# Optimization experiments

Hardware: AMD Instinct MI355X
Metric: run time of the kernel (lower is better)

Reference implementation:

```python
import jax, jax.numpy as jnp
import numpy as np

N_NODES = 50000
N_EDGES = 800000
N_FEAT = 256


def setup_inputs() -> dict:
    key = jax.random.key(0)
    k_h, k_src, k_dst, k_w1, k_w2 = jax.random.split(key, 5)
    h = jax.random.normal(k_h, (N_NODES, N_FEAT), dtype=jnp.float32)
    src = jax.random.randint(k_src, (N_EDGES,), 0, N_NODES, dtype=jnp.int32)
    dst = jax.random.randint(k_dst, (N_EDGES,), 0, N_NODES, dtype=jnp.int32)
    # Kaiming-uniform-ish init like nn.Linear defaults
    b1 = 1.0 / np.sqrt(2 * N_FEAT)
    b2 = 1.0 / np.sqrt(N_FEAT)
    W1_w = jax.random.uniform(k_w1, (N_FEAT, 2 * N_FEAT), dtype=jnp.float32, minval=-b1, maxval=b1)
    W1_b = jnp.zeros((N_FEAT,), dtype=jnp.float32)
    W2_w = jax.random.uniform(k_w2, (1, N_FEAT), dtype=jnp.float32, minval=-b2, maxval=b2)
    W2_b = jnp.zeros((1,), dtype=jnp.float32)
    return {"h": h, "src": src, "dst": dst, "W1_w": W1_w, "W1_b": W1_b, "W2_w": W2_w, "W2_b": W2_b}


def reference(h, src, dst, W1_w, W1_b, W2_w, W2_b):
    # Gather per-edge endpoint features and concat along feature dim: [E, 2F]
    e = jnp.concatenate([h[src], h[dst]], axis=-1)
    # 2-layer MLP: Linear -> ReLU -> Linear, squeeze to per-edge score [E]
    hid = jax.nn.relu(e @ W1_w.T + W1_b)          # [E, F]
    score = (hid @ W2_w.T + W2_b)[:, 0]            # [E]
    return score
```

## Files before the change

### kernel.cpp

```cpp
#include <hip/hip_runtime.h>

#define F 256
#define TWO_F 512
#define BM 128
#define BN 64
#define BK 64

typedef __attribute__((ext_vector_type(8))) short short8;
typedef __attribute__((ext_vector_type(4))) float float4v;

static __device__ __forceinline__ unsigned short f2bf(float f) {
    unsigned u = __float_as_uint(f);
    u += 0x7FFFu + ((u >> 16) & 1u);
    return (unsigned short)(u >> 16);
}
static __device__ __forceinline__ unsigned pack2(float lo, float hi) {
    unsigned a = __float_as_uint(lo) + 0x8000u;
    unsigned b = __float_as_uint(hi) + 0x8000u;
    return __builtin_amdgcn_perm(b, a, 0x07060302u);
}
static __device__ __forceinline__ float blo(unsigned u) { return __uint_as_float(u << 16); }
static __device__ __forceinline__ float rawf(unsigned u) { return __uint_as_float(u); }

__global__ __launch_bounds__(256) void prep_kernel(
    const float* __restrict__ h, const float* __restrict__ W1,
    unsigned short* __restrict__ hb, unsigned short* __restrict__ Wb, int M)
{
    int i = blockIdx.x * blockDim.x + threadIdx.x;
    if (i < M * 128) {
        int m = i >> 7;
        int kp = (i & 127) * 2;
        float2 v = *(const float2*)(h + (size_t)m * F + kp);
        unsigned pk = pack2(v.x, v.y);
        int ksw = ((kp & 63) + (m & 7) * 8) & 63;
        *(unsigned*)(hb + (size_t)m * F + (kp & ~63) + ksw) = pk;
    }
    if (i < TWO_F * F) {
        int n = i >> 8;
        int k = i & 255;
        float v = W1[(n & 255) * TWO_F + ((n >> 8) << 8) + k];
        int kin_sw = ((k & 63) + (n & 7) * 8) & 63;
        Wb[n * F + (k & ~63) + kin_sw] = f2bf(v);
    }
}

__global__ __launch_bounds__(256, 4) void gemm_kernel(
    const unsigned short* __restrict__ hb, const unsigned short* __restrict__ Wb,
    const float* __restrict__ b1v, unsigned short* __restrict__ C, int M)
{
    __shared__ unsigned short sA[BM * BK];
    __shared__ unsigned short sB[BN * BK];

    const int ib = blockIdx.x;
    const int r8 = ib & 7;
    const int q  = ib >> 3;
    const int by = q & 7;
    const int bx = (q >> 3) * 8 + r8;
    const int bm = bx * BM;
    if (bm >= M) return;
    const int bn = by * BN;

    const int tid  = threadIdx.x;
    const int lane = tid & 63;
    const int wid  = tid >> 6;
    const int st_r = lane >> 3;
    const int st_k = (lane & 7) * 8;
    const int quad = lane >> 4;
    const int l15  = lane & 15;
    const int rot  = (l15 & 7) * 8;

    float4v acc[2][4];
    #pragma unroll
    for (int i = 0; i < 2; ++i)
        #pragma unroll
        for (int j = 0; j < 4; ++j) acc[i][j] = (float4v)(0.f);

    for (int k0 = 0; k0 < F; k0 += BK) {
        #pragma unroll
        for (int p = 0; p < 4; ++p) {
            int r = wid * 32 + p * 8;
            int am = bm + r + st_r; if (am > M - 1) am = M - 1;
            const unsigned short* ga = hb + (size_t)am * F + k0 + st_k;
            __builtin_amdgcn_global_load_lds(
                (const __attribute__((address_space(1))) unsigned int*)ga,
                (__attribute__((address_space(3))) unsigned int*)&sA[r * BK],
                16, 0, 0);
        }
        #pragma unroll
        for (int p = 0; p < 2; ++p) {
            int r = wid * 16 + p * 8;
            const unsigned short* gb = Wb + (size_t)(bn + r + st_r) * F + k0 + st_k;
            __builtin_amdgcn_global_load_lds(
                (const __attribute__((address_space(1))) unsigned int*)gb,
                (__attribute__((address_space(3))) unsigned int*)&sB[r * BK],
                16, 0, 0);
        }
        __syncthreads();

        #pragma unroll
        for (int ks = 0; ks < 2; ++ks) {
            const int koff = (ks * 32 + quad * 8 + rot) & 63;
            short8 afr[2], bfr[4];
            #pragma unroll
            for (int mt = 0; mt < 2; ++mt)
                afr[mt] = *(const short8*)&sA[(wid * 32 + mt * 16 + l15) * BK + koff];
            #pragma unroll
            for (int nt = 0; nt < 4; ++nt)
                bfr[nt] = *(const short8*)&sB[(nt * 16 + l15) * BK + koff];
            #pragma unroll
            for (int mt = 0; mt < 2; ++mt)
                #pragma unroll
                for (int nt = 0; nt < 4; ++nt)
                    acc[mt][nt] = __builtin_amdgcn_mfma_f32_16x16x32_bf16(
                        afr[mt], bfr[nt], acc[mt][nt], 0, 0, 0);
        }
        __syncthreads();
    }

    float bias[4];
    #pragma unroll
    for (int nt = 0; nt < 4; ++nt) {
        int n = bn + nt * 16 + l15;
        bias[nt] = (n < F) ? b1v[n] : 0.f;
    }
    #pragma unroll
    for (int mt = 0; mt < 2; ++mt) {
        int gm0 = bm + wid * 32 + mt * 16 + quad * 4;
        #pragma unroll
        for (int rr = 0; rr < 4; ++rr) {
            int gm = gm0 + rr;
            if (gm < M) {
                unsigned short* cp = C + (size_t)gm * TWO_F + bn + l15;
                #pragma unroll
                for (int nt = 0; nt < 4; ++nt)
                    cp[nt * 16] = f2bf(acc[mt][nt][rr] + bias[nt]);
            }
        }
    }
}

__global__ __launch_bounds__(256) void edge_kernel(
    const unsigned short* __restrict__ C,
    const int* __restrict__ src, const int* __restrict__ dst,
    const float* __restrict__ w2,
    const float* __restrict__ b2, float* __restrict__ out, int E)
{
    const int lane = threadIdx.x & 31;
    const int g = blockIdx.x * 8 + (threadIdx.x >> 5);
    const int e0 = g * 2;
    if (e0 >= E) return;
    const int s0 = src[e0], d0 = dst[e0];
    const int s1 = src[e0 + 1], d1 = dst[e0 + 1];

    uint4 av0 = *(const uint4*)(C + (size_t)s0 * TWO_F + lane * 8);
    uint4 bv0 = *(const uint4*)(C + (size_t)d0 * TWO_F + F + lane * 8);
    uint4 av1 = *(const uint4*)(C + (size_t)s1 * TWO_F + lane * 8);
    uint4 bv1 = *(const uint4*)(C + (size_t)d1 * TWO_F + F + lane * 8);
    float4 w0 = *(const float4*)(w2 + lane * 8);
    float4 w1 = *(const float4*)(w2 + lane * 8 + 4);

    float sum0, sum1;
    sum0  = w0.x * fmaxf(blo(av0.x) + blo(bv0.x), 0.f);
    sum0 += w0.y * fmaxf(rawf(av0.x) + rawf(bv0.x), 0.f);
    sum0 += w0.z * fmaxf(blo(av0.y) + blo(bv0.y), 0.f);
    sum0 += w0.w * fmaxf(rawf(av0.y) + rawf(bv0.y), 0.f);
    sum0 += w1.x * fmaxf(blo(av0.z) + blo(bv0.z), 0.f);
    sum0 += w1.y * fmaxf(rawf(av0.z) + rawf(bv0.z), 0.f);
    sum0 += w1.z * fmaxf(blo(av0.w) + blo(bv0.w), 0.f);
    sum0 += w1.w * fmaxf(rawf(av0.w) + rawf(bv0.w), 0.f);

    sum1  = w0.x * fmaxf(blo(av1.x) + blo(bv1.x), 0.f);
    sum1 += w0.y * fmaxf(rawf(av1.x) + rawf(bv1.x), 0.f);
    sum1 += w0.z * fmaxf(blo(av1.y) + blo(bv1.y), 0.f);
    sum1 += w0.w * fmaxf(rawf(av1.y) + rawf(bv1.y), 0.f);
    sum1 += w1.x * fmaxf(blo(av1.z) + blo(bv1.z), 0.f);
    sum1 += w1.y * fmaxf(rawf(av1.z) + rawf(bv1.z), 0.f);
    sum1 += w1.z * fmaxf(blo(av1.w) + blo(bv1.w), 0.f);
    sum1 += w1.w * fmaxf(rawf(av1.w) + rawf(bv1.w), 0.f);

    #pragma unroll
    for (int off = 16; off > 0; off >>= 1) {
        sum0 += __shfl_down(sum0, off, 32);
        sum1 += __shfl_down(sum1, off, 32);
    }

    if (lane == 0) {
        float b = b2[0];
        out[e0]     = sum0 + b;
        out[e0 + 1] = sum1 + b;
    }
}

extern "C" void kernel_launch(void* const* d_in, const int* in_sizes, int n_in,
                              void* d_out, int out_size, void* d_ws, size_t ws_size,
                              hipStream_t stream) {
    const float* h    = (const float*)d_in[0];
    const int*   src  = (const int*)d_in[1];
    const int*   dst  = (const int*)d_in[2];
    const float* W1_w = (const float*)d_in[3];
    const float* W1_b = (const float*)d_in[4];
    const float* W2_w = (const float*)d_in[5];
    const float* W2_b = (const float*)d_in[6];
    float* out = (float*)d_out;

    const int M = in_sizes[0] / F;
    const int E = in_sizes[1];

    unsigned short* Wb = (unsigned short*)d_ws;
    unsigned short* hb = (unsigned short*)((char*)d_ws + 512 * 1024);
    unsigned short* C  = (unsigned short*)((char*)d_ws + 512 * 1024 + 26 * 1024 * 1024);

    int prep_threads = M * 128 > TWO_F * F ? M * 128 : TWO_F * F;
    prep_kernel<<<(prep_threads + 255) / 256, 256, 0, stream>>>(h, W1_w, hb, Wb, M);

    int nbx = ((M + BM - 1) / BM + 7) / 8 * 8;
    gemm_kernel<<<nbx * 8, 256, 0, stream>>>(hb, Wb, W1_b, C, M);

    edge_kernel<<<(E / 2 + 7) / 8, 256, 0, stream>>>(C, src, dst, W2_w, W2_b, out, E);
}
```

Measured before the change: 226.7 us.

## Load full K into LDS with 64x64 tiles and a 2x2 wave layout in GEMM

The node GEMM now uses 64x64 output tiles and stages the entire K=256 extent of both A and B into LDS in one shot, instead of looping over K in 64-wide slabs with two barriers per slab. Waves are arranged 2x2 over the tile, and each wave computes a 32x32 sub-tile. The goal is fewer barriers and more blocks, which should hide latency better. In exchange, each block needs 64 KB of LDS, which caps occupancy at 2 blocks per CU, and the MFMA-to-load ratio per wave is smaller.

```diff
diff --git a/kernel.cpp b/kernel.cpp
--- a/kernel.cpp
+++ b/kernel.cpp
@@ -2,9 +2,6 @@
 
 #define F 256
 #define TWO_F 512
-#define BM 128
-#define BN 64
-#define BK 64
 
 typedef __attribute__((ext_vector_type(8))) short short8;
 typedef __attribute__((ext_vector_type(4))) float float4v;
@@ -44,95 +41,85 @@
     }
 }
 
-__global__ __launch_bounds__(256, 4) void gemm_kernel(
+__global__ __launch_bounds__(256, 2) void gemm_kernel(
     const unsigned short* __restrict__ hb, const unsigned short* __restrict__ Wb,
     const float* __restrict__ b1v, unsigned short* __restrict__ C, int M)
 {
-    __shared__ unsigned short sA[BM * BK];
-    __shared__ unsigned short sB[BN * BK];
+    __shared__ unsigned short sA[64 * F];
+    __shared__ unsigned short sB[64 * F];
 
     const int ib = blockIdx.x;
     const int r8 = ib & 7;
-    const int q  = ib >> 3;
-    const int by = q & 7;
-    const int bx = (q >> 3) * 8 + r8;
-    const int bm = bx * BM;
+    const int nb = (ib >> 3) & 7;
+    const int mq = ib >> 6;
+    const int mchunk = mq * 8 + r8;
+    const int bm = mchunk * 64;
     if (bm >= M) return;
-    const int bn = by * BN;
+    const int bn = nb * 64;
 
     const int tid  = threadIdx.x;
     const int lane = tid & 63;
     const int wid  = tid >> 6;
-    const int st_r = lane >> 3;
-    const int st_k = (lane & 7) * 8;
+    const int wm   = wid >> 1;
+    const int wn   = wid & 1;
     const int quad = lane >> 4;
     const int l15  = lane & 15;
     const int rot  = (l15 & 7) * 8;
 
-    float4v acc[2][4];
-    #pragma unroll
-    for (int i = 0; i < 2; ++i)
-        #pragma unroll
-        for (int j = 0; j < 4; ++j) acc[i][j] = (float4v)(0.f);
-
-    for (int k0 = 0; k0 < F; k0 += BK) {
-        #pragma unroll
-        for (int p = 0; p < 4; ++p) {
-            int r = wid * 32 + p * 8;
-            int am = bm + r + st_r; if (am > M - 1) am = M - 1;
-            const unsigned short* ga = hb + (size_t)am * F + k0 + st_k;
-            __builtin_amdgcn_global_load_lds(
-                (const __attribute__((address_space(1))) unsigned int*)ga,
-                (__attribute__((address_space(3))) unsigned int*)&sA[r * BK],
-                16, 0, 0);
-        }
-        #pragma unroll
-        for (int p = 0; p < 2; ++p) {
-            int r = wid * 16 + p * 8;
-            const unsigned short* gb = Wb + (size_t)(bn + r + st_r) * F + k0 + st_k;
-            __builtin_amdgcn_global_load_lds(
-                (const __attribute__((address_space(1))) unsigned int*)gb,
-                (__attribute__((address_space(3))) unsigned int*)&sB[r * BK],
-                16, 0, 0);
-        }
-        __syncthreads();
-
-        #pragma unroll
-        for (int ks = 0; ks < 2; ++ks) {
-            const int koff = (ks * 32 + quad * 8 + rot) & 63;
-            short8 afr[2], bfr[4];
+    #pragma unroll
+    for (int p = 0; p < 8; ++p) {
+        int idx = wid * 8 + p;
+        int am = bm + 2 * idx; if (am > M - 2) am = M - 2;
+        const unsigned short* ga = hb + (size_t)am * F + lane * 8;
+        __builtin_amdgcn_global_load_lds(
+            (const __attribute__((address_space(1))) unsigned int*)ga,
+            (__attribute__((address_space(3))) unsigned int*)&sA[(2 * idx) * F],
+            16, 0, 0);
+        const unsigned short* gb = Wb + (size_t)(bn + 2 * idx) * F + lane * 8;
+        __builtin_amdgcn_global_load_lds(
+            (const __attribute__((address_space(1))) unsigned int*)gb,
+            (__attribute__((address_space(3))) unsigned int*)&sB[(2 * idx) * F],
+            16, 0, 0);
+    }
+    __syncthreads();
+
+    float4v acc[2][2];
+    acc[0][0] = acc[0][1] = acc[1][0] = acc[1][1] = (float4v)(0.f);
+
+    #pragma unroll
+    for (int ks = 0; ks < 8; ++ks) {
+        const int off = ((ks >> 1) << 6) + ((((ks & 1) << 5) + (quad << 3) + rot) & 63);
+        short8 afr[2], bfr[2];
+        #pragma unroll
+        for (int mt = 0; mt < 2; ++mt)
+            afr[mt] = *(const short8*)&sA[(wm * 32 + mt * 16 + l15) * F + off];
+        #pragma unroll
+        for (int nt = 0; nt < 2; ++nt)
+            bfr[nt] = *(const short8*)&sB[(wn * 32 + nt * 16 + l15) * F + off];
+        #pragma unroll
+        for (int mt = 0; mt < 2; ++mt)
             #pragma unroll
-            for (int mt = 0; mt < 2; ++mt)
-                afr[mt] = *(const short8*)&sA[(wid * 32 + mt * 16 + l15) * BK + koff];
-            #pragma unroll
-            for (int nt = 0; nt < 4; ++nt)
-                bfr[nt] = *(const short8*)&sB[(nt * 16 + l15) * BK + koff];
-            #pragma unroll
-            for (int mt = 0; mt < 2; ++mt)
-                #pragma unroll
-                for (int nt = 0; nt < 4; ++nt)
-                    acc[mt][nt] = __builtin_amdgcn_mfma_f32_16x16x32_bf16(
-                        afr[mt], bfr[nt], acc[mt][nt], 0, 0, 0);
-        }
-        __syncthreads();
-    }
-
-    float bias[4];
-    #pragma unroll
-    for (int nt = 0; nt < 4; ++nt) {
-        int n = bn + nt * 16 + l15;
+            for (int nt = 0; nt < 2; ++nt)
+                acc[mt][nt] = __builtin_amdgcn_mfma_f32_16x16x32_bf16(
+                    afr[mt], bfr[nt], acc[mt][nt], 0, 0, 0);
+    }
+
+    float bias[2];
+    #pragma unroll
+    for (int nt = 0; nt < 2; ++nt) {
+        int n = bn + wn * 32 + nt * 16 + l15;
         bias[nt] = (n < F) ? b1v[n] : 0.f;
     }
     #pragma unroll
     for (int mt = 0; mt < 2; ++mt) {
-        int gm0 = bm + wid * 32 + mt * 16 + quad * 4;
+        int gm0 = bm + wm * 32 + mt * 16 + quad * 4;
         #pragma unroll
         for (int rr = 0; rr < 4; ++rr) {
             int gm = gm0 + rr;
             if (gm < M) {
-                unsigned short* cp = C + (size_t)gm * TWO_F + bn + l15;
+                unsigned short* cp = C + (size_t)gm * TWO_F + bn + wn * 32 + l15;
                 #pragma unroll
-                for (int nt = 0; nt < 4; ++nt)
+                for (int nt = 0; nt < 2; ++nt)
                     cp[nt * 16] = f2bf(acc[mt][nt][rr] + bias[nt]);
             }
         }
@@ -213,8 +200,8 @@
     int prep_threads = M * 128 > TWO_F * F ? M * 128 : TWO_F * F;
     prep_kernel<<<(prep_threads + 255) / 256, 256, 0, stream>>>(h, W1_w, hb, Wb, M);
 
-    int nbx = ((M + BM - 1) / BM + 7) / 8 * 8;
-    gemm_kernel<<<nbx * 8, 256, 0, stream>>>(hb, Wb, W1_b, C, M);
+    int mq = (((M + 63) / 64) + 7) / 8;
+    gemm_kernel<<<mq * 64, 256, 0, stream>>>(hb, Wb, W1_b, C, M);
 
     edge_kernel<<<(E / 2 + 7) / 8, 256, 0, stream>>>(C, src, dst, W2_w, W2_b, out, E);
 }
```

After: 245.0 us. +8.1%, slower.

## Sort edges by source node via counting sort before edge gather

Applied to the files above, without the earlier changes.

Adds a histogram, a single-block prefix scan and an atomic scatter that bucket the edges by source node into a grouped (src, dst, idx) array, reusing the hb workspace once the GEMM has consumed it. The edge kernel then walks edges in source order so repeated source-row gathers from C hit cache, and it scatters scores back to their original indices. In exchange it adds three kernel launches, global atomics, a serial single-block scan over 50k bins, and an extra pass reading and writing 800k edge records.

```diff
diff --git a/kernel.cpp b/kernel.cpp
--- a/kernel.cpp
+++ b/kernel.cpp
@@ -24,7 +24,8 @@
 
 __global__ __launch_bounds__(256) void prep_kernel(
     const float* __restrict__ h, const float* __restrict__ W1,
-    unsigned short* __restrict__ hb, unsigned short* __restrict__ Wb, int M)
+    unsigned short* __restrict__ hb, unsigned short* __restrict__ Wb,
+    int* __restrict__ bins, int M)
 {
     int i = blockIdx.x * blockDim.x + threadIdx.x;
     if (i < M * 128) {
@@ -42,6 +43,36 @@
         int kin_sw = ((k & 63) + (n & 7) * 8) & 63;
         Wb[n * F + (k & ~63) + kin_sw] = f2bf(v);
     }
+    if (i < M) bins[i] = 0;
+}
+
+__global__ __launch_bounds__(256) void hist_kernel(
+    const int* __restrict__ src, int* __restrict__ bins, int E)
+{
+    int i = blockIdx.x * blockDim.x + threadIdx.x;
+    if (i < E) atomicAdd(&bins[src[i]], 1);
+}
+
+__global__ __launch_bounds__(1024) void scan_kernel(
+    const int* __restrict__ bins, int* __restrict__ cursor, int M)
+{
+    __shared__ int part[1024];
+    const int t = threadIdx.x;
+    const int chunk = (M + 1023) / 1024;
+    const int lo = t * chunk;
+    const int hi = (lo + chunk < M) ? lo + chunk : M;
+    int s = 0;
+    for (int i = lo; i < hi; ++i) s += bins[i];
+    part[t] = s;
+    __syncthreads();
+    for (int off = 1; off < 1024; off <<= 1) {
+        int v = (t >= off) ? part[t - off] : 0;
+        __syncthreads();
+        part[t] += v;
+        __syncthreads();
+    }
+    int run = (t > 0) ? part[t - 1] : 0;
+    for (int i = lo; i < hi; ++i) { cursor[i] = run; run += bins[i]; }
 }
 
 __global__ __launch_bounds__(256, 4) void gemm_kernel(
@@ -139,9 +170,20 @@
     }
 }
 
+__global__ __launch_bounds__(256) void scatter_kernel(
+    const int* __restrict__ src, const int* __restrict__ dst,
+    int* __restrict__ cursor, int4* __restrict__ grouped, int E)
+{
+    int i = blockIdx.x * blockDim.x + threadIdx.x;
+    if (i >= E) return;
+    int s = src[i];
+    int pos = atomicAdd(&cursor[s], 1);
+    grouped[pos] = make_int4(s, dst[i], i, 0);
+}
+
 __global__ __launch_bounds__(256) void edge_kernel(
     const unsigned short* __restrict__ C,
-    const int* __restrict__ src, const int* __restrict__ dst,
+    const int4* __restrict__ grouped,
     const float* __restrict__ w2,
     const float* __restrict__ b2, float* __restrict__ out, int E)
 {
@@ -149,13 +191,13 @@
     const int g = blockIdx.x * 8 + (threadIdx.x >> 5);
     const int e0 = g * 2;
     if (e0 >= E) return;
-    const int s0 = src[e0], d0 = dst[e0];
-    const int s1 = src[e0 + 1], d1 = dst[e0 + 1];
-
-    uint4 av0 = *(const uint4*)(C + (size_t)s0 * TWO_F + lane * 8);
-    uint4 bv0 = *(const uint4*)(C + (size_t)d0 * TWO_F + F + lane * 8);
-    uint4 av1 = *(const uint4*)(C + (size_t)s1 * TWO_F + lane * 8);
-    uint4 bv1 = *(const uint4*)(C + (size_t)d1 * TWO_F + F + lane * 8);
+    int4 t0 = grouped[e0];
+    int4 t1 = grouped[e0 + 1];
+
+    uint4 av0 = *(const uint4*)(C + (size_t)t0.x * TWO_F + lane * 8);
+    uint4 bv0 = *(const uint4*)(C + (size_t)t0.y * TWO_F + F + lane * 8);
+    uint4 av1 = *(const uint4*)(C + (size_t)t1.x * TWO_F + lane * 8);
+    uint4 bv1 = *(const uint4*)(C + (size_t)t1.y * TWO_F + F + lane * 8);
     float4 w0 = *(const float4*)(w2 + lane * 8);
     float4 w1 = *(const float4*)(w2 + lane * 8 + 4);
 
@@ -186,8 +228,8 @@
 
     if (lane == 0) {
         float b = b2[0];
-        out[e0]     = sum0 + b;
-        out[e0 + 1] = sum1 + b;
+        out[t0.z] = sum0 + b;
+        out[t1.z] = sum1 + b;
     }
 }
 
@@ -206,15 +248,24 @@
     const int M = in_sizes[0] / F;
     const int E = in_sizes[1];
 
-    unsigned short* Wb = (unsigned short*)d_ws;
-    unsigned short* hb = (unsigned short*)((char*)d_ws + 512 * 1024);
-    unsigned short* C  = (unsigned short*)((char*)d_ws + 512 * 1024 + 26 * 1024 * 1024);
+    char* ws = (char*)d_ws;
+    unsigned short* Wb = (unsigned short*)ws;
+    unsigned short* hb = (unsigned short*)(ws + 512 * 1024);
+    int4* grouped      = (int4*)(ws + 512 * 1024);
+    int* bins          = (int*)(ws + 512 * 1024 + (size_t)M * F * 2);
+    int* cursor        = bins + M;
+    unsigned short* C  = (unsigned short*)(ws + 512 * 1024 + 26 * 1024 * 1024);
 
     int prep_threads = M * 128 > TWO_F * F ? M * 128 : TWO_F * F;
-    prep_kernel<<<(prep_threads + 255) / 256, 256, 0, stream>>>(h, W1_w, hb, Wb, M);
+    prep_kernel<<<(prep_threads + 255) / 256, 256, 0, stream>>>(h, W1_w, hb, Wb, bins, M);
+
+    hist_kernel<<<(E + 255) / 256, 256, 0, stream>>>(src, bins, E);
+    scan_kernel<<<1, 1024, 0, stream>>>(bins, cursor, M);
 
     int nbx = ((M + BM - 1) / BM + 7) / 8 * 8;
     gemm_kernel<<<nbx * 8, 256, 0, stream>>>(hb, Wb, W1_b, C, M);
 
-    edge_kernel<<<(E / 2 + 7) / 8, 256, 0, stream>>>(C, src, dst, W2_w, W2_b, out, E);
-}
+    scatter_kernel<<<(E + 255) / 256, 256, 0, stream>>>(src, dst, cursor, grouped, E);
+
+    edge_kernel<<<(E / 2 + 7) / 8, 256, 0, stream>>>(C, grouped, W2_w, W2_b, out, E);
+}
```

Result: slower. 358.3 us (+58.0%).

## Bucket edges by destination range and map bucket blocks per XCD for locality

Applied to the files above, without the earlier changes.

Adds count, prefix and scatter kernels that group edges into 8 buckets by destination node range, packing src and dst into 16-bit fields with the original edge index. The edge kernel assigns each bucket to blocks with the same blockIdx&7, presumably so each XCD's L2 serves a compact slice of the dst half of C, and uses nontemporal loads for the random src rows. This adds three extra launches plus atomics and an extra pass over src/dst, and reuses the hb workspace for the grouped array after the GEMM. The 16-bit packing assumes node count below 65536, and Bmax assumes bucket sizes stay within E/8 plus slack.

```diff
diff --git a/kernel.cpp b/kernel.cpp
--- a/kernel.cpp
+++ b/kernel.cpp
@@ -8,6 +8,7 @@
 
 typedef __attribute__((ext_vector_type(8))) short short8;
 typedef __attribute__((ext_vector_type(4))) float float4v;
+typedef __attribute__((ext_vector_type(4))) unsigned uint4v;
 
 static __device__ __forceinline__ unsigned short f2bf(float f) {
     unsigned u = __float_as_uint(f);
@@ -22,9 +23,14 @@
 static __device__ __forceinline__ float blo(unsigned u) { return __uint_as_float(u << 16); }
 static __device__ __forceinline__ float rawf(unsigned u) { return __uint_as_float(u); }
 
+#define MT_GCNT 0
+#define MT_START 8
+#define MT_CURSOR 17
+
 __global__ __launch_bounds__(256) void prep_kernel(
     const float* __restrict__ h, const float* __restrict__ W1,
-    unsigned short* __restrict__ hb, unsigned short* __restrict__ Wb, int M)
+    unsigned short* __restrict__ hb, unsigned short* __restrict__ Wb,
+    int* __restrict__ meta, int M)
 {
     int i = blockIdx.x * blockDim.x + threadIdx.x;
     if (i < M * 128) {
@@ -41,6 +47,33 @@
         float v = W1[(n & 255) * TWO_F + ((n >> 8) << 8) + k];
         int kin_sw = ((k & 63) + (n & 7) * 8) & 63;
         Wb[n * F + (k & ~63) + kin_sw] = f2bf(v);
+    }
+    if (i < 8) meta[MT_GCNT + i] = 0;
+}
+
+__global__ __launch_bounds__(256) void count_kernel(
+    const int* __restrict__ dst, int* __restrict__ meta, int E, int NB)
+{
+    __shared__ int lcnt[8];
+    const int t = threadIdx.x;
+    if (t < 8) lcnt[t] = 0;
+    __syncthreads();
+    int i = blockIdx.x * 256 + t;
+    if (i < E) atomicAdd(&lcnt[dst[i] / NB], 1);
+    __syncthreads();
+    if (t < 8 && lcnt[t] > 0) atomicAdd(&meta[MT_GCNT + t], lcnt[t]);
+}
+
+__global__ void cursor_kernel(int* __restrict__ meta)
+{
+    if (threadIdx.x == 0) {
+        int run = 0;
+        for (int x = 0; x < 8; ++x) {
+            meta[MT_START + x] = run;
+            meta[MT_CURSOR + x] = run;
+            run += meta[MT_GCNT + x];
+        }
+        meta[MT_START + 8] = run;
     }
 }
 
@@ -139,23 +172,55 @@
     }
 }
 
+__global__ __launch_bounds__(256) void scatter_kernel(
+    const int* __restrict__ src, const int* __restrict__ dst,
+    int* __restrict__ meta, int2* __restrict__ grouped, int E, int NB)
+{
+    __shared__ int lcnt[8];
+    __shared__ int lbase[8];
+    const int t = threadIdx.x;
+    if (t < 8) lcnt[t] = 0;
+    __syncthreads();
+    int i = blockIdx.x * 256 + t;
+    int b = 0, rank = 0, s = 0, d = 0;
+    bool ok = (i < E);
+    if (ok) {
+        s = src[i]; d = dst[i];
+        b = d / NB;
+        rank = atomicAdd(&lcnt[b], 1);
+    }
+    __syncthreads();
+    if (t < 8 && lcnt[t] > 0) lbase[t] = atomicAdd(&meta[MT_CURSOR + t], lcnt[t]);
+    __syncthreads();
+    if (ok) {
+        int pos = lbase[b] + rank;
+        grouped[pos] = make_int2((s << 16) | d, i);
+    }
+}
+
 __global__ __launch_bounds__(256) void edge_kernel(
     const unsigned short* __restrict__ C,
-    const int* __restrict__ src, const int* __restrict__ dst,
+    const int2* __restrict__ grouped, const int* __restrict__ meta,
     const float* __restrict__ w2,
-    const float* __restrict__ b2, float* __restrict__ out, int E)
-{
+    const float* __restrict__ b2, float* __restrict__ out)
+{
+    const int x  = blockIdx.x & 7;
+    const int bi = blockIdx.x >> 3;
+    const int stx = meta[MT_START + x];
+    const int endx = meta[MT_START + x + 1];
     const int lane = threadIdx.x & 31;
-    const int g = blockIdx.x * 8 + (threadIdx.x >> 5);
-    const int e0 = g * 2;
-    if (e0 >= E) return;
-    const int s0 = src[e0], d0 = dst[e0];
-    const int s1 = src[e0 + 1], d1 = dst[e0 + 1];
-
-    uint4 av0 = *(const uint4*)(C + (size_t)s0 * TWO_F + lane * 8);
-    uint4 bv0 = *(const uint4*)(C + (size_t)d0 * TWO_F + F + lane * 8);
-    uint4 av1 = *(const uint4*)(C + (size_t)s1 * TWO_F + lane * 8);
-    uint4 bv1 = *(const uint4*)(C + (size_t)d1 * TWO_F + F + lane * 8);
+    const int e0 = stx + bi * 16 + (threadIdx.x >> 5) * 2;
+    if (e0 >= endx) return;
+    int2 t0 = grouped[e0];
+    bool has1 = (e0 + 1 < endx);
+    int2 t1 = has1 ? grouped[e0 + 1] : t0;
+    const int s0 = ((unsigned)t0.x) >> 16, d0 = t0.x & 0xFFFF;
+    const int s1 = ((unsigned)t1.x) >> 16, d1 = t1.x & 0xFFFF;
+
+    uint4v av0 = __builtin_nontemporal_load((const uint4v*)(C + (size_t)s0 * TWO_F + lane * 8));
+    uint4v bv0 = *(const uint4v*)(C + (size_t)d0 * TWO_F + F + lane * 8);
+    uint4v av1 = __builtin_nontemporal_load((const uint4v*)(C + (size_t)s1 * TWO_F + lane * 8));
+    uint4v bv1 = *(const uint4v*)(C + (size_t)d1 * TWO_F + F + lane * 8);
     float4 w0 = *(const float4*)(w2 + lane * 8);
     float4 w1 = *(const float4*)(w2 + lane * 8 + 4);
 
@@ -186,8 +251,8 @@
 
     if (lane == 0) {
         float b = b2[0];
-        out[e0]     = sum0 + b;
-        out[e0 + 1] = sum1 + b;
+        out[t0.y] = sum0 + b;
+        if (has1) out[t1.y] = sum1 + b;
     }
 }
 
@@ -205,16 +270,26 @@
 
     const int M = in_sizes[0] / F;
     const int E = in_sizes[1];
-
-    unsigned short* Wb = (unsigned short*)d_ws;
-    unsigned short* hb = (unsigned short*)((char*)d_ws + 512 * 1024);
-    unsigned short* C  = (unsigned short*)((char*)d_ws + 512 * 1024 + 26 * 1024 * 1024);
+    const int NB = (M + 7) / 8;
+
+    char* ws = (char*)d_ws;
+    unsigned short* Wb = (unsigned short*)ws;
+    unsigned short* hb = (unsigned short*)(ws + 512 * 1024);
+    int2* grouped      = (int2*)(ws + 512 * 1024);
+    int* meta          = (int*)(ws + 512 * 1024 + (size_t)M * F * 2);
+    unsigned short* C  = (unsigned short*)(ws + 512 * 1024 + 26 * 1024 * 1024);
 
     int prep_threads = M * 128 > TWO_F * F ? M * 128 : TWO_F * F;
-    prep_kernel<<<(prep_threads + 255) / 256, 256, 0, stream>>>(h, W1_w, hb, Wb, M);
+    prep_kernel<<<(prep_threads + 255) / 256, 256, 0, stream>>>(h, W1_w, hb, Wb, meta, M);
+
+    count_kernel<<<(E + 255) / 256, 256, 0, stream>>>(dst, meta, E, NB);
+    cursor_kernel<<<1, 64, 0, stream>>>(meta);
 
     int nbx = ((M + BM - 1) / BM + 7) / 8 * 8;
     gemm_kernel<<<nbx * 8, 256, 0, stream>>>(hb, Wb, W1_b, C, M);
 
-    edge_kernel<<<(E / 2 + 7) / 8, 256, 0, stream>>>(C, src, dst, W2_w, W2_b, out, E);
-}
+    scatter_kernel<<<(E + 255) / 256, 256, 0, stream>>>(src, dst, meta, grouped, E, NB);
+
+    int Bmax = (E / 8 + 16384 + 15) / 16;
+    edge_kernel<<<8 * Bmax, 256, 0, stream>>>(C, grouped, meta, W2_w, W2_b, out);
+}
```

Result: slower. 301.6 us (+33.0%).
